# Performance work log

Measured on AMD Instinct MI355X. Metric: run time of the kernel, lower is better.

The kernel has to match this reference:

```python
import jax, jax.numpy as jnp
import numpy as np

B, N, M, C = 2, 8192, 1024, 1152  # batch, dense points, centers, feature dim
K = 3                              # three_nn interpolation
EPS = 1e-8


def setup_inputs() -> dict:
    key = jax.random.key(0)
    k1, k2, k3 = jax.random.split(key, 3)
    xyz = jax.random.normal(k1, (B, N, 3), dtype=jnp.float32)      # query points
    center = jax.random.normal(k2, (B, M, 3), dtype=jnp.float32)   # center coords (already permuted to B,M,3)
    feats = jax.random.normal(k3, (B, C, M), dtype=jnp.float32)    # backbone features at centers
    return {"xyz": xyz, "center": center, "feats": feats}


def _interpolate(xyz, center, feats):
    # Squared pairwise distances [B, N, M] (PointNet++ three_nn uses squared dists).
    d2 = (jnp.sum(xyz * xyz, axis=-1, keepdims=True)
          + jnp.sum(center * center, axis=-1)[:, None, :]
          - 2.0 * jnp.einsum('bnd,bmd->bnm', xyz, center))
    neg_top, idx = jax.lax.top_k(-d2, K)          # 3 nearest centers per point
    dist = -neg_top                                # [B, N, K] squared distances
    recip = 1.0 / (dist + EPS)
    weight = recip / jnp.sum(recip, axis=-1, keepdims=True)  # [B, N, K]
    fm = jnp.transpose(feats, (0, 2, 1))           # [B, M, C]
    batch_idx = jnp.arange(B)[:, None, None]       # broadcast gather over batch
    gathered = fm[batch_idx, idx]                  # [B, N, K, C]
    out = jnp.einsum('bnkc,bnk->bcn', gathered, weight)  # [B, C, N]
    return out


def reference(xyz, center, feats):
    return _interpolate(xyz, center, feats)
```

## Files before the change

kernel.cpp:

```cpp
#include <hip/hip_runtime.h>
#include <cstdint>

#define B_ 2
#define N_ 8192
#define M_ 1024
#define C_ 1152
#define EPS_ 1e-8f
#define NT 32
#define CHUNK 128
#define NBN (N_ / NT)
#define NBC (C_ / CHUNK)

typedef float f32x4 __attribute__((ext_vector_type(4)));

__device__ __forceinline__ unsigned short f2bf(float f) {
    unsigned u = __float_as_uint(f);
    u += 0x7fffu + ((u >> 16) & 1u);
    return (unsigned short)(u >> 16);
}
__device__ __forceinline__ float bf2f(unsigned short h) {
    return __uint_as_float(((unsigned)h) << 16);
}

__global__ __launch_bounds__(256) void k_transpose(const float* __restrict__ feats,
                                                   unsigned short* __restrict__ fm) {
    __shared__ float tile[64][65];
    int m0 = blockIdx.x * 64;
    int c0 = blockIdx.y * 64;
    int b  = blockIdx.z;
    int tx = threadIdx.x;
    int ty = threadIdx.y;
    const float* src = feats + ((size_t)b * C_ + c0) * M_ + m0;
#pragma unroll
    for (int j = 0; j < 16; ++j) {
        int cl = ty + 4 * j;
        tile[cl][tx] = __builtin_nontemporal_load(&src[(size_t)cl * M_ + tx]);
    }
    __syncthreads();
    unsigned short* dst = fm + ((size_t)b * M_ + m0) * C_ + c0;
#pragma unroll
    for (int j = 0; j < 16; ++j) {
        int ml = ty + 4 * j;
        dst[(size_t)ml * C_ + tx] = f2bf(tile[tx][ml]);
    }
}

__device__ __forceinline__ unsigned long long pack_di(float d, int m) {
    unsigned u = __float_as_uint(d);
    unsigned s = (unsigned)((int)u >> 31);
    u ^= (s | 0x80000000u);
    return ((unsigned long long)u << 32) | (unsigned)m;
}
__device__ __forceinline__ float unpack_d(unsigned long long k) {
    unsigned u = (unsigned)(k >> 32);
    unsigned s = (unsigned)((int)u >> 31);
    u ^= (~s | 0x80000000u);
    return __uint_as_float(u);
}
__device__ __forceinline__ void kinsert(unsigned long long p,
        unsigned long long& k0, unsigned long long& k1, unsigned long long& k2) {
    unsigned long long t;
    bool c0 = p < k0; t = c0 ? k0 : p; k0 = c0 ? p : k0; p = t;
    bool c1 = p < k1; t = c1 ? k1 : p; k1 = c1 ? p : k1; p = t;
    k2 = (p < k2) ? p : k2;
}
__device__ __forceinline__ unsigned long long shfl_xor_u64(unsigned long long v, int off) {
    int lo = __shfl_xor((int)(unsigned)v, off);
    int hi = __shfl_xor((int)(unsigned)(v >> 32), off);
    return ((unsigned long long)(unsigned)hi << 32) | (unsigned)lo;
}

#define NC 16
#define PTS 16

__global__ __launch_bounds__(256) void k_threenn(const float* __restrict__ xyz,
                                                 const float* __restrict__ center,
                                                 int* __restrict__ idx_ws,
                                                 float* __restrict__ w_ws) {
    __shared__ float4 sc[M_];
    int b  = blockIdx.y;
    int n0 = blockIdx.x * PTS;
    int t  = threadIdx.x;
    for (int i = t; i < M_; i += 256) {
        float cx = center[((size_t)b * M_ + i) * 3 + 0];
        float cy = center[((size_t)b * M_ + i) * 3 + 1];
        float cz = center[((size_t)b * M_ + i) * 3 + 2];
        float cc = __fadd_rn(__fadd_rn(__fmul_rn(cx, cx), __fmul_rn(cy, cy)),
                             __fmul_rn(cz, cz));
        sc[i] = make_float4(cx, cy, cz, cc);
    }
    __syncthreads();

    int p = t >> 4;
    int c = t & 15;
    int n = n0 + p;
    float x = xyz[((size_t)b * N_ + n) * 3 + 0];
    float y = xyz[((size_t)b * N_ + n) * 3 + 1];
    float z = xyz[((size_t)b * N_ + n) * 3 + 2];
    float xx = __fadd_rn(__fadd_rn(__fmul_rn(x, x), __fmul_rn(y, y)),
                         __fmul_rn(z, z));

    unsigned long long k0 = ~0ull, k1 = ~0ull, k2 = ~0ull;
#pragma unroll 4
    for (int it = 0; it < M_ / NC; ++it) {
        int m = c + it * NC;
        float4 v = sc[m];
        float dot = __fmaf_rn(z, v.z, __fmaf_rn(y, v.y, __fmul_rn(x, v.x)));
        float d   = __fsub_rn(__fadd_rn(xx, v.w), __fmul_rn(2.0f, dot));
        kinsert(pack_di(d, m), k0, k1, k2);
    }
#pragma unroll
    for (int off = 1; off <= 8; off <<= 1) {
        unsigned long long e0 = shfl_xor_u64(k0, off);
        unsigned long long e1 = shfl_xor_u64(k1, off);
        unsigned long long e2 = shfl_xor_u64(k2, off);
        kinsert(e0, k0, k1, k2);
        kinsert(e1, k0, k1, k2);
        kinsert(e2, k0, k1, k2);
    }
    if (c == 0) {
        float r0 = 1.0f / __fadd_rn(unpack_d(k0), EPS_);
        float r1 = 1.0f / __fadd_rn(unpack_d(k1), EPS_);
        float r2 = 1.0f / __fadd_rn(unpack_d(k2), EPS_);
        float s  = __fadd_rn(__fadd_rn(r0, r1), r2);
        size_t base = ((size_t)b * N_ + n) * 3;
        idx_ws[base + 0] = (int)(unsigned)k0;
        idx_ws[base + 1] = (int)(unsigned)k1;
        idx_ws[base + 2] = (int)(unsigned)k2;
        w_ws[base + 0] = r0 / s; w_ws[base + 1] = r1 / s; w_ws[base + 2] = r2 / s;
    }
}

__global__ __launch_bounds__(256) void k_interp(const unsigned short* __restrict__ fm,
                                                const int* __restrict__ idx_ws,
                                                const float* __restrict__ w_ws,
                                                float* __restrict__ out) {
    __shared__ float T[NT][CHUNK + 1];
    __shared__ int   sbase[NT][3];
    __shared__ float sw[NT][3];
    int flat = blockIdx.x;
    int slot = flat & 7;
    int b    = slot >> 2;
    int idx  = (flat >> 3) * 4 + (slot & 3);
    int n0   = (idx & (NBN - 1)) * NT;
    int c0   = (idx >> 8) * CHUNK;
    int t    = threadIdx.x;
    if (t < NT) {
        size_t ib = ((size_t)b * N_ + n0 + t) * 3;
#pragma unroll
        for (int k = 0; k < 3; ++k) {
            sbase[t][k] = (b * M_ + idx_ws[ib + k]) * C_;
            sw[t][k]    = w_ws[ib + k];
        }
    }
    __syncthreads();
    int wave = t >> 6;
    int lane = t & 63;
    int half = lane >> 5;
    int cl   = (lane & 31) * 4;
#pragma unroll
    for (int pp = 0; pp < 4; ++pp) {
        int p = pp * 8 + wave * 2 + half;
        float w0 = sw[p][0], w1 = sw[p][1], w2 = sw[p][2];
        const ushort4 a0 = *(const ushort4*)(fm + sbase[p][0] + c0 + cl);
        const ushort4 a1 = *(const ushort4*)(fm + sbase[p][1] + c0 + cl);
        const ushort4 a2 = *(const ushort4*)(fm + sbase[p][2] + c0 + cl);
        T[p][cl + 0] = __fmaf_rn(bf2f(a2.x), w2, __fmaf_rn(bf2f(a1.x), w1, __fmul_rn(bf2f(a0.x), w0)));
        T[p][cl + 1] = __fmaf_rn(bf2f(a2.y), w2, __fmaf_rn(bf2f(a1.y), w1, __fmul_rn(bf2f(a0.y), w0)));
        T[p][cl + 2] = __fmaf_rn(bf2f(a2.z), w2, __fmaf_rn(bf2f(a1.z), w1, __fmul_rn(bf2f(a0.z), w0)));
        T[p][cl + 3] = __fmaf_rn(bf2f(a2.w), w2, __fmaf_rn(bf2f(a1.w), w1, __fmul_rn(bf2f(a0.w), w0)));
    }
    __syncthreads();
    int p4  = (t & 7) * 4;
    int ccb = t >> 3;
#pragma unroll
    for (int r = 0; r < 4; ++r) {
        int cc = r * 32 + ccb;
        f32x4 v = { T[p4 + 0][cc], T[p4 + 1][cc], T[p4 + 2][cc], T[p4 + 3][cc] };
        __builtin_nontemporal_store(v,
            (f32x4*)&out[((size_t)b * C_ + c0 + cc) * N_ + n0 + p4]);
    }
}

extern "C" void kernel_launch(void* const* d_in, const int* in_sizes, int n_in,
                              void* d_out, int out_size, void* d_ws, size_t ws_size,
                              hipStream_t stream) {
    const float* xyz    = (const float*)d_in[0];
    const float* center = (const float*)d_in[1];
    const float* feats  = (const float*)d_in[2];
    float* out = (float*)d_out;

    char*           ws     = (char*)d_ws;
    unsigned short* fm     = (unsigned short*)ws;
    int*            idx_ws = (int*)(ws + (size_t)B_ * M_ * C_ * 2);
    float*          w_ws   = (float*)(ws + (size_t)B_ * M_ * C_ * 2 + (size_t)B_ * N_ * 3 * 4);

    k_transpose<<<dim3(M_ / 64, C_ / 64, B_), dim3(64, 4), 0, stream>>>(feats, fm);
    k_threenn <<<dim3(N_ / PTS, B_), 256, 0, stream>>>(xyz, center, idx_ws, w_ws);
    k_interp  <<<NBN * NBC * B_, 256, 0, stream>>>(fm, idx_ws, w_ws, out);
}
```

Measured before the change: 41.95 us.

## Assign one wave per query point and use float/int top-3 insertion

The three-NN kernel now gives each 64-lane wave a single query point, so each lane scans 16 centers instead of 64, and it handles 4 points per block instead of 16. The packed 64-bit key top-3 is replaced by separate float distance and int index registers with a branchless three-way insert, and the cross-lane merge uses a lexicographic tie-break. The aim is a shorter serial scan per lane and cheaper 32-bit compares. In exchange there are four times as many blocks, each reloading all centers into shared memory, and a longer shuffle reduction over six steps.

```diff
diff --git a/kernel.cpp b/kernel.cpp
--- a/kernel.cpp
+++ b/kernel.cpp
@@ -45,38 +45,31 @@
     }
 }
 
-__device__ __forceinline__ unsigned long long pack_di(float d, int m) {
-    unsigned u = __float_as_uint(d);
-    unsigned s = (unsigned)((int)u >> 31);
-    u ^= (s | 0x80000000u);
-    return ((unsigned long long)u << 32) | (unsigned)m;
+__device__ __forceinline__ void ins3(float d, int i,
+        float& d0, int& i0, float& d1, int& i1, float& d2, int& i2) {
+    bool b0 = d < d0;
+    bool b1 = d < d1;
+    bool b2 = d < d2;
+    d2 = b1 ? d1 : (b2 ? d : d2);   i2 = b1 ? i1 : (b2 ? i : i2);
+    d1 = b0 ? d0 : (b1 ? d : d1);   i1 = b0 ? i0 : (b1 ? i : i1);
+    d0 = b0 ? d  : d0;              i0 = b0 ? i  : i0;
 }
-__device__ __forceinline__ float unpack_d(unsigned long long k) {
-    unsigned u = (unsigned)(k >> 32);
-    unsigned s = (unsigned)((int)u >> 31);
-    u ^= (~s | 0x80000000u);
-    return __uint_as_float(u);
-}
-__device__ __forceinline__ void kinsert(unsigned long long p,
-        unsigned long long& k0, unsigned long long& k1, unsigned long long& k2) {
-    unsigned long long t;
-    bool c0 = p < k0; t = c0 ? k0 : p; k0 = c0 ? p : k0; p = t;
-    bool c1 = p < k1; t = c1 ? k1 : p; k1 = c1 ? p : k1; p = t;
-    k2 = (p < k2) ? p : k2;
-}
-__device__ __forceinline__ unsigned long long shfl_xor_u64(unsigned long long v, int off) {
-    int lo = __shfl_xor((int)(unsigned)v, off);
-    int hi = __shfl_xor((int)(unsigned)(v >> 32), off);
-    return ((unsigned long long)(unsigned)hi << 32) | (unsigned)lo;
+__device__ __forceinline__ void ins3lex(float d, int i,
+        float& d0, int& i0, float& d1, int& i1, float& d2, int& i2) {
+    bool b0 = (d < d0) || (d == d0 && i < i0);
+    bool b1 = (d < d1) || (d == d1 && i < i1);
+    bool b2 = (d < d2) || (d == d2 && i < i2);
+    d2 = b1 ? d1 : (b2 ? d : d2);   i2 = b1 ? i1 : (b2 ? i : i2);
+    d1 = b0 ? d0 : (b1 ? d : d1);   i1 = b0 ? i0 : (b1 ? i : i1);
+    d0 = b0 ? d  : d0;              i0 = b0 ? i  : i0;
 }
 
-#define NC 16
-#define PTS 16
+#define PTS 4
 
-__global__ __launch_bounds__(256) void k_threenn(const float* __restrict__ xyz,
-                                                 const float* __restrict__ center,
-                                                 int* __restrict__ idx_ws,
-                                                 float* __restrict__ w_ws) {
+__global__ __launch_bounds__(256, 8) void k_threenn(const float* __restrict__ xyz,
+                                                    const float* __restrict__ center,
+                                                    int* __restrict__ idx_ws,
+                                                    float* __restrict__ w_ws) {
     __shared__ float4 sc[M_];
     int b  = blockIdx.y;
     int n0 = blockIdx.x * PTS;
@@ -91,42 +84,41 @@
     }
     __syncthreads();
 
-    int p = t >> 4;
-    int c = t & 15;
-    int n = n0 + p;
+    int w = t >> 6;
+    int l = t & 63;
+    int n = n0 + w;
     float x = xyz[((size_t)b * N_ + n) * 3 + 0];
     float y = xyz[((size_t)b * N_ + n) * 3 + 1];
     float z = xyz[((size_t)b * N_ + n) * 3 + 2];
     float xx = __fadd_rn(__fadd_rn(__fmul_rn(x, x), __fmul_rn(y, y)),
                          __fmul_rn(z, z));
 
-    unsigned long long k0 = ~0ull, k1 = ~0ull, k2 = ~0ull;
+    float d0 = __builtin_inff(), d1 = __builtin_inff(), d2 = __builtin_inff();
+    int   i0 = 0x7fffffff,  i1 = 0x7fffffff,  i2 = 0x7fffffff;
 #pragma unroll 4
-    for (int it = 0; it < M_ / NC; ++it) {
-        int m = c + it * NC;
+    for (int it = 0; it < M_ / 64; ++it) {
+        int m = l + it * 64;
         float4 v = sc[m];
         float dot = __fmaf_rn(z, v.z, __fmaf_rn(y, v.y, __fmul_rn(x, v.x)));
         float d   = __fsub_rn(__fadd_rn(xx, v.w), __fmul_rn(2.0f, dot));
-        kinsert(pack_di(d, m), k0, k1, k2);
+        ins3(d, m, d0, i0, d1, i1, d2, i2);
     }
 #pragma unroll
-    for (int off = 1; off <= 8; off <<= 1) {
-        unsigned long long e0 = shfl_xor_u64(k0, off);
-        unsigned long long e1 = shfl_xor_u64(k1, off);
-        unsigned long long e2 = shfl_xor_u64(k2, off);
-        kinsert(e0, k0, k1, k2);
-        kinsert(e1, k0, k1, k2);
-        kinsert(e2, k0, k1, k2);
+    for (int off = 1; off <= 32; off <<= 1) {
+        float e0 = __shfl_xor(d0, off); int j0 = __shfl_xor(i0, off);
+        float e1 = __shfl_xor(d1, off); int j1 = __shfl_xor(i1, off);
+        float e2 = __shfl_xor(d2, off); int j2 = __shfl_xor(i2, off);
+        ins3lex(e0, j0, d0, i0, d1, i1, d2, i2);
+        ins3lex(e1, j1, d0, i0, d1, i1, d2, i2);
+        ins3lex(e2, j2, d0, i0, d1, i1, d2, i2);
     }
-    if (c == 0) {
-        float r0 = 1.0f / __fadd_rn(unpack_d(k0), EPS_);
-        float r1 = 1.0f / __fadd_rn(unpack_d(k1), EPS_);
-        float r2 = 1.0f / __fadd_rn(unpack_d(k2), EPS_);
+    if (l == 0) {
+        float r0 = 1.0f / __fadd_rn(d0, EPS_);
+        float r1 = 1.0f / __fadd_rn(d1, EPS_);
+        float r2 = 1.0f / __fadd_rn(d2, EPS_);
         float s  = __fadd_rn(__fadd_rn(r0, r1), r2);
         size_t base = ((size_t)b * N_ + n) * 3;
-        idx_ws[base + 0] = (int)(unsigned)k0;
-        idx_ws[base + 1] = (int)(unsigned)k1;
-        idx_ws[base + 2] = (int)(unsigned)k2;
+        idx_ws[base + 0] = i0; idx_ws[base + 1] = i1; idx_ws[base + 2] = i2;
         w_ws[base + 0] = r0 / s; w_ws[base + 1] = r1 / s; w_ws[base + 2] = r2 / s;
     }
 }
```

Result: slower. 47.31 us (+12.8%).
